# Optimization experiments

Hardware: AMD Instinct MI355X
Metric: run time of the kernel (lower is better)

Reference implementation:

```python
import jax, jax.numpy as jnp
import numpy as np

B, F_G, F_L, F_INT = 2, 64, 64, 32
D = H = W = 64
BN_EPS = 1e-5


def setup_inputs() -> dict:
    key = jax.random.key(0)
    ks = jax.random.split(key, 8)
    g = jax.random.normal(ks[0], (B, F_G, D, H, W), dtype=jnp.float32)
    x = jax.random.normal(ks[1], (B, F_L, D, H, W), dtype=jnp.float32)
    # Gating MLP (1x1x1 convs on pooled features == dense layers)
    w1 = jax.random.normal(ks[2], (F_INT, F_G + F_L), dtype=jnp.float32) * (1.0 / np.sqrt(F_G + F_L))
    b1 = jnp.zeros((F_INT,), dtype=jnp.float32)
    w2 = jax.random.normal(ks[3], (F_G * F_L, F_INT), dtype=jnp.float32) * (1.0 / np.sqrt(F_INT))
    b2 = jnp.zeros((F_G * F_L,), dtype=jnp.float32)
    # psi: Conv3d(F_l, 1, k=1) + BatchNorm3d(1) (inference-mode stats)
    psi_w = jax.random.normal(ks[4], (F_L,), dtype=jnp.float32) * (1.0 / np.sqrt(F_L))
    psi_b = jnp.zeros((1,), dtype=jnp.float32)
    bn_gamma = jnp.ones((1,), dtype=jnp.float32)
    bn_beta = jnp.zeros((1,), dtype=jnp.float32)
    bn_mean = jnp.zeros((1,), dtype=jnp.float32)
    bn_var = jnp.ones((1,), dtype=jnp.float32)
    return {"g": g, "x": x, "w1": w1, "b1": b1, "w2": w2, "b2": b2,
            "psi_w": psi_w, "psi_b": psi_b, "bn_gamma": bn_gamma,
            "bn_beta": bn_beta, "bn_mean": bn_mean, "bn_var": bn_var}


def reference(g, x, w1, b1, w2, b2, psi_w, psi_b, bn_gamma, bn_beta, bn_mean, bn_var):
    # Global average pool of cat([g, x]) -> [B, F_g+F_l]
    pooled = jnp.concatenate([jnp.mean(g, axis=(2, 3, 4)), jnp.mean(x, axis=(2, 3, 4))], axis=1)
    h = jax.nn.relu(pooled @ w1.T + b1)                       # [B, F_int]
    dw = jax.nn.sigmoid(h @ w2.T + b2).reshape(B, F_G, F_L)   # dynamic weights [B, F_g, F_l]
    # attended[b,l,d,h,w] = sum_g g[b,g,d,h,w] * dw[b,g,l]  (batched GEMM, no 6D blow-up)
    attended = jnp.einsum('bgdhw,bgl->bldhw', g, dw)
    # psi: 1x1x1 conv to 1 channel + BN + sigmoid
    s = jnp.einsum('bldhw,l->bdhw', attended, psi_w) + psi_b[0]
    s = (s - bn_mean[0]) * (bn_gamma[0] / jnp.sqrt(bn_var[0] + BN_EPS)) + bn_beta[0]
    return x * jax.nn.sigmoid(s)[:, None]                     # [B, F_l, D, H, W]
```

## Files before the change

### kernel.cpp

```cpp
#include <hip/hip_runtime.h>
#include <math.h>

#define SPATIAL (64*64*64)
#define SPATIAL4 (SPATIAL/4)
#define NCH 64
#define BN_EPS 1e-5f

#define NBLK   2048
#define NTILE  65536
#define GTILES 32768

typedef float v4f __attribute__((ext_vector_type(4)));

__global__ __launch_bounds__(256) void mean_kernel(const float* __restrict__ g,
                                                   const float* __restrict__ x,
                                                   float* __restrict__ wpart) {
    int b    = blockIdx.x;
    int tid  = threadIdx.x;
    int lane = tid & 63, wave = tid >> 6;
    const v4f* g4 = (const v4f*)g;
    const v4f* x4 = (const v4f*)x;

    #pragma unroll 4
    for (int k = 0; k < 32; ++k) {
        int T = k * NBLK + b;
        const v4f* src = (T < GTILES) ? (g4 + (size_t)T * 256)
                                      : (x4 + (size_t)(T - GTILES) * 256);
        v4f v = src[tid];
        float s = (v.x + v.y) + (v.z + v.w);
        #pragma unroll
        for (int off = 32; off > 0; off >>= 1)
            s += __shfl_down(s, off, 64);
        if (lane == 0) wpart[T * 4 + wave] = s;
    }
}

__global__ __launch_bounds__(256) void fold_kernel(const float* __restrict__ wpart,
                                                   float* __restrict__ pooled) {
    int ch  = blockIdx.x;
    int tid = threadIdx.x;
    const v4f* src = (const v4f*)(wpart + (size_t)ch * 1024);
    v4f v = src[tid];
    float s = (v.x + v.y) + (v.z + v.w);
    #pragma unroll
    for (int off = 32; off > 0; off >>= 1)
        s += __shfl_down(s, off, 64);
    __shared__ float ws[4];
    if ((tid & 63) == 0) ws[tid >> 6] = s;
    __syncthreads();
    if (tid == 0) {
        float tot = (ws[0] + ws[1]) + (ws[2] + ws[3]);
        int pi = (ch < 128) ? ((ch >> 6) * 128 + (ch & 63))
                            : (((ch - 128) >> 6) * 128 + 64 + ((ch - 128) & 63));
        pooled[pi] = tot * (1.0f / SPATIAL);
    }
}

__global__ __launch_bounds__(64) void mlp_kernel(const float* __restrict__ pooled,
                           const float* __restrict__ w1, const float* __restrict__ b1,
                           const float* __restrict__ w2, const float* __restrict__ b2,
                           const float* __restrict__ psi_w, const float* __restrict__ psi_b,
                           const float* __restrict__ bn_gamma, const float* __restrict__ bn_beta,
                           const float* __restrict__ bn_mean, const float* __restrict__ bn_var,
                           float* __restrict__ coef) {
    __shared__ float p[256];
    __shared__ float h[32];
    int tid = threadIdx.x;
    int blk = blockIdx.x;
    int b = blk >> 6, gc = blk & 63;

    #pragma unroll
    for (int i = tid; i < 256; i += 64) p[i] = pooled[i];
    __syncthreads();
    if (tid < 32) {
        float acc = b1[tid];
        const float* wr = w1 + tid * 128;
        #pragma unroll 4
        for (int k = 0; k < 128; ++k) acc += p[b * 128 + k] * wr[k];
        h[tid] = fmaxf(acc, 0.f);
    }
    __syncthreads();
    const float4* wr = (const float4*)(w2 + (size_t)(gc * 64 + tid) * 32);
    float z = b2[gc * 64 + tid];
    #pragma unroll
    for (int j = 0; j < 8; ++j) {
        float4 wv = wr[j];
        z += h[4*j] * wv.x + h[4*j+1] * wv.y + h[4*j+2] * wv.z + h[4*j+3] * wv.w;
    }
    float sig = 1.f / (1.f + expf(-z));
    float val = sig * psi_w[tid];
    #pragma unroll
    for (int off = 32; off > 0; off >>= 1)
        val += __shfl_down(val, off, 64);
    float scale = bn_gamma[0] * rsqrtf(bn_var[0] + BN_EPS);
    if (tid == 0) coef[b * 64 + gc] = val * scale;
    if (blk == 0 && tid == 0)
        coef[128] = (psi_b[0] - bn_mean[0]) * scale + bn_beta[0];
}

__device__ __forceinline__ void fma4(v4f& a, v4f v, float c) {
    a.x += v.x * c; a.y += v.y * c; a.z += v.z * c; a.w += v.w * c;
}

__global__ __launch_bounds__(256, 8) void apply_kernel(const float* __restrict__ g,
                                                       const float* __restrict__ x,
                                                       const float* __restrict__ coef,
                                                       float* __restrict__ out) {
    int t    = threadIdx.x;
    int pos  = t & 63;
    int grp  = t >> 6;
    int blk  = blockIdx.x;
    int batch = blk >> 10;
    int base4 = (blk & 1023) * 64 + pos;
    size_t bOff = (size_t)batch * NCH * SPATIAL4;

    const v4f* g4 = (const v4f*)g;
    const v4f* x4 = (const v4f*)x;
    v4f* o4 = (v4f*)out;

    const v4f* cfv = (const v4f*)(coef + batch * NCH + grp * 16);
    const v4f* gp = g4 + bOff + (size_t)(grp * 16) * SPATIAL4 + base4;

    v4f acc0 = {0.f,0.f,0.f,0.f}, acc1 = {0.f,0.f,0.f,0.f};
    #pragma unroll
    for (int bq = 0; bq < 4; ++bq) {
        v4f cv = cfv[bq];
        v4f v0 = __builtin_nontemporal_load(gp + (size_t)(4*bq + 0) * SPATIAL4);
        v4f v1 = __builtin_nontemporal_load(gp + (size_t)(4*bq + 1) * SPATIAL4);
        v4f v2 = __builtin_nontemporal_load(gp + (size_t)(4*bq + 2) * SPATIAL4);
        v4f v3 = __builtin_nontemporal_load(gp + (size_t)(4*bq + 3) * SPATIAL4);
        fma4(acc0, v0, cv.x);
        fma4(acc1, v1, cv.y);
        fma4(acc0, v2, cv.z);
        fma4(acc1, v3, cv.w);
    }
    v4f acc = {acc0.x + acc1.x, acc0.y + acc1.y, acc0.z + acc1.z, acc0.w + acc1.w};

    __shared__ v4f red[4][64];
    if (grp != 0) red[grp][pos] = acc;
    __syncthreads();
    if (grp == 0) {
        v4f r1 = red[1][pos], r2 = red[2][pos], r3 = red[3][pos];
        float d = coef[128];
        v4f s;
        s.x = 1.f / (1.f + expf(-(acc.x + r1.x + r2.x + r3.x + d)));
        s.y = 1.f / (1.f + expf(-(acc.y + r1.y + r2.y + r3.y + d)));
        s.z = 1.f / (1.f + expf(-(acc.z + r1.z + r2.z + r3.z + d)));
        s.w = 1.f / (1.f + expf(-(acc.w + r1.w + r2.w + r3.w + d)));
        red[0][pos] = s;
    }
    __syncthreads();
    v4f s = red[0][pos];

    const v4f* xp = x4 + bOff + (size_t)(grp * 16) * SPATIAL4 + base4;
    v4f*       op = o4 + bOff + (size_t)(grp * 16) * SPATIAL4 + base4;
    #pragma unroll 4
    for (int l = 0; l < 16; ++l) {
        v4f xv = xp[(size_t)l * SPATIAL4];
        v4f ov = {xv.x * s.x, xv.y * s.y, xv.z * s.z, xv.w * s.w};
        __builtin_nontemporal_store(ov, op + (size_t)l * SPATIAL4);
    }
}

extern "C" void kernel_launch(void* const* d_in, const int* in_sizes, int n_in,
                              void* d_out, int out_size, void* d_ws, size_t ws_size,
                              hipStream_t stream) {
    const float* g        = (const float*)d_in[0];
    const float* x        = (const float*)d_in[1];
    const float* w1       = (const float*)d_in[2];
    const float* b1       = (const float*)d_in[3];
    const float* w2       = (const float*)d_in[4];
    const float* b2       = (const float*)d_in[5];
    const float* psi_w    = (const float*)d_in[6];
    const float* psi_b    = (const float*)d_in[7];
    const float* bn_gamma = (const float*)d_in[8];
    const float* bn_beta  = (const float*)d_in[9];
    const float* bn_mean  = (const float*)d_in[10];
    const float* bn_var   = (const float*)d_in[11];
    float* out = (float*)d_out;
    float* ws  = (float*)d_ws;

    float* wpart  = ws;
    float* pooled = ws + NTILE * 4;
    float* coef   = pooled + 256;

    mean_kernel<<<NBLK, 256, 0, stream>>>(g, x, wpart);
    fold_kernel<<<256, 256, 0, stream>>>(wpart, pooled);
    mlp_kernel<<<128, 64, 0, stream>>>(pooled, w1, b1, w2, b2, psi_w, psi_b,
                                       bn_gamma, bn_beta, bn_mean, bn_var, coef);
    apply_kernel<<<2048, 256, 0, stream>>>(g, x, coef, out);
}
```

Measured before the change: 378.1 us.

## Restructure mean reduction to match apply_kernel access pattern with deep per-thread loads

The mean kernel now has each block cover a spatial chunk across 16 channels per wave for both g and x, with 32 independent loads issued per thread and butterfly reductions afterwards. This mirrors the apply kernel's access pattern, which may improve L2/MALL reuse of g and x by the later kernel, and gives more memory-level parallelism. Partial sums are stored in a [chunk][feature] layout, and the fold kernel now does strided gathers over 1024 chunks per feature. The change uses more registers per thread and makes the fold kernel's reads uncoalesced.

```diff
diff --git a/kernel.cpp b/kernel.cpp
--- a/kernel.cpp
+++ b/kernel.cpp
@@ -6,42 +6,67 @@
 #define NCH 64
 #define BN_EPS 1e-5f
 
-#define NBLK   2048
-#define NTILE  65536
-#define GTILES 32768
-
 typedef float v4f __attribute__((ext_vector_type(4)));
 
 __global__ __launch_bounds__(256) void mean_kernel(const float* __restrict__ g,
                                                    const float* __restrict__ x,
                                                    float* __restrict__ wpart) {
-    int b    = blockIdx.x;
-    int tid  = threadIdx.x;
-    int lane = tid & 63, wave = tid >> 6;
-    const v4f* g4 = (const v4f*)g;
-    const v4f* x4 = (const v4f*)x;
-
-    #pragma unroll 4
-    for (int k = 0; k < 32; ++k) {
-        int T = k * NBLK + b;
-        const v4f* src = (T < GTILES) ? (g4 + (size_t)T * 256)
-                                      : (x4 + (size_t)(T - GTILES) * 256);
-        v4f v = src[tid];
-        float s = (v.x + v.y) + (v.z + v.w);
-        #pragma unroll
-        for (int off = 32; off > 0; off >>= 1)
-            s += __shfl_down(s, off, 64);
-        if (lane == 0) wpart[T * 4 + wave] = s;
+    int t     = threadIdx.x;
+    int lane  = t & 63;
+    int grp   = t >> 6;
+    int blk   = blockIdx.x;
+    int batch = blk >> 10;
+    int chunk = blk & 1023;
+    int base4 = chunk * 64 + lane;
+    size_t bOff = (size_t)batch * NCH * SPATIAL4;
+
+    const v4f* gp = (const v4f*)g + bOff + (size_t)(grp * 16) * SPATIAL4 + base4;
+    const v4f* xp = (const v4f*)x + bOff + (size_t)(grp * 16) * SPATIAL4 + base4;
+
+    float ga0,ga1,ga2,ga3,ga4,ga5,ga6,ga7,ga8,ga9,ga10,ga11,ga12,ga13,ga14,ga15;
+    float xa0,xa1,xa2,xa3,xa4,xa5,xa6,xa7,xa8,xa9,xa10,xa11,xa12,xa13,xa14,xa15;
+#define HS(v) ((v.x + v.y) + (v.z + v.w))
+#define LDG(n) { v4f v = __builtin_nontemporal_load(gp + (size_t)(n) * SPATIAL4); ga##n = HS(v); }
+#define LDX(n) { v4f v = xp[(size_t)(n) * SPATIAL4]; xa##n = HS(v); }
+    LDG(0) LDG(1) LDG(2) LDG(3) LDG(4) LDG(5) LDG(6) LDG(7)
+    LDG(8) LDG(9) LDG(10) LDG(11) LDG(12) LDG(13) LDG(14) LDG(15)
+    LDX(0) LDX(1) LDX(2) LDX(3) LDX(4) LDX(5) LDX(6) LDX(7)
+    LDX(8) LDX(9) LDX(10) LDX(11) LDX(12) LDX(13) LDX(14) LDX(15)
+#undef LDG
+#undef LDX
+#undef HS
+
+#define RED(v) { v += __shfl_xor(v, 32, 64); v += __shfl_xor(v, 16, 64); \
+                 v += __shfl_xor(v,  8, 64); v += __shfl_xor(v,  4, 64); \
+                 v += __shfl_xor(v,  2, 64); v += __shfl_xor(v,  1, 64); }
+    RED(ga0) RED(ga1) RED(ga2) RED(ga3) RED(ga4) RED(ga5) RED(ga6) RED(ga7)
+    RED(ga8) RED(ga9) RED(ga10) RED(ga11) RED(ga12) RED(ga13) RED(ga14) RED(ga15)
+    RED(xa0) RED(xa1) RED(xa2) RED(xa3) RED(xa4) RED(xa5) RED(xa6) RED(xa7)
+    RED(xa8) RED(xa9) RED(xa10) RED(xa11) RED(xa12) RED(xa13) RED(xa14) RED(xa15)
+#undef RED
+
+    if (lane == 0) {
+        float* wr = wpart + (size_t)chunk * 256 + batch * 64 + grp * 16;
+        wr[0]=ga0;  wr[1]=ga1;  wr[2]=ga2;  wr[3]=ga3;
+        wr[4]=ga4;  wr[5]=ga5;  wr[6]=ga6;  wr[7]=ga7;
+        wr[8]=ga8;  wr[9]=ga9;  wr[10]=ga10; wr[11]=ga11;
+        wr[12]=ga12; wr[13]=ga13; wr[14]=ga14; wr[15]=ga15;
+        float* wr2 = wr + 128;
+        wr2[0]=xa0;  wr2[1]=xa1;  wr2[2]=xa2;  wr2[3]=xa3;
+        wr2[4]=xa4;  wr2[5]=xa5;  wr2[6]=xa6;  wr2[7]=xa7;
+        wr2[8]=xa8;  wr2[9]=xa9;  wr2[10]=xa10; wr2[11]=xa11;
+        wr2[12]=xa12; wr2[13]=xa13; wr2[14]=xa14; wr2[15]=xa15;
     }
 }
 
 __global__ __launch_bounds__(256) void fold_kernel(const float* __restrict__ wpart,
                                                    float* __restrict__ pooled) {
-    int ch  = blockIdx.x;
+    int f   = blockIdx.x;
     int tid = threadIdx.x;
-    const v4f* src = (const v4f*)(wpart + (size_t)ch * 1024);
-    v4f v = src[tid];
-    float s = (v.x + v.y) + (v.z + v.w);
+    float s = 0.f;
+    #pragma unroll
+    for (int k = 0; k < 4; ++k)
+        s += wpart[(size_t)(k * 256 + tid) * 256 + f];
     #pragma unroll
     for (int off = 32; off > 0; off >>= 1)
         s += __shfl_down(s, off, 64);
@@ -50,8 +75,9 @@
     __syncthreads();
     if (tid == 0) {
         float tot = (ws[0] + ws[1]) + (ws[2] + ws[3]);
-        int pi = (ch < 128) ? ((ch >> 6) * 128 + (ch & 63))
-                            : (((ch - 128) >> 6) * 128 + 64 + ((ch - 128) & 63));
+        int pi;
+        if (f < 128) { int b = f >> 6, c = f & 63; pi = b * 128 + c; }
+        else         { int b = (f - 128) >> 6, c = f & 63; pi = b * 128 + 64 + c; }
         pooled[pi] = tot * (1.0f / SPATIAL);
     }
 }
@@ -181,10 +207,10 @@
     float* ws  = (float*)d_ws;
 
     float* wpart  = ws;
-    float* pooled = ws + NTILE * 4;
+    float* pooled = ws + 1024 * 256;
     float* coef   = pooled + 256;
 
-    mean_kernel<<<NBLK, 256, 0, stream>>>(g, x, wpart);
+    mean_kernel<<<2048, 256, 0, stream>>>(g, x, wpart);
     fold_kernel<<<256, 256, 0, stream>>>(wpart, pooled);
     mlp_kernel<<<128, 64, 0, stream>>>(pooled, w1, b1, w2, b2, psi_w, psi_b,
                                        bn_gamma, bn_beta, bn_mean, bn_var, coef);
```

Result: no change. 373.1 us (-1.3%).
